# Kernel tuning notes

Measured on AMD Instinct MI355X. Metric: run time of the kernel, lower is better.

## Reference

```python
import jax, jax.numpy as jnp
import numpy as np

B, S, D = 2, 2048, 1024
H, DH = 16, 64
INNER = H * DH  # 1024
FF = 4 * D
WINDOW = 128
EPS = 1e-5
SCALE = DH ** -0.5


def setup_inputs() -> dict:
    key = jax.random.key(0)
    ks = jax.random.split(key, 8)
    s = lambda fan_in: 1.0 / np.sqrt(fan_in)
    return {
        "x": jax.random.normal(ks[0], (B, S, D), dtype=jnp.float32),
        "ln1_g": jnp.ones((D,), jnp.float32),
        "ln1_b": jnp.zeros((D,), jnp.float32),
        "w_qkv": jax.random.uniform(ks[1], (3 * INNER, D), jnp.float32, -s(D), s(D)),
        "w_out": jax.random.uniform(ks[2], (D, INNER), jnp.float32, -s(INNER), s(INNER)),
        "b_out": jnp.zeros((D,), jnp.float32),
        "ln2_g": jnp.ones((D,), jnp.float32),
        "ln2_b": jnp.zeros((D,), jnp.float32),
        "w_ff1": jax.random.uniform(ks[3], (FF, D), jnp.float32, -s(D), s(D)),
        "b_ff1": jnp.zeros((FF,), jnp.float32),
        "w_ff2": jax.random.uniform(ks[4], (D, FF), jnp.float32, -s(FF), s(FF)),
        "b_ff2": jnp.zeros((D,), jnp.float32),
    }


def _layernorm(x, g, b):
    mu = jnp.mean(x, axis=-1, keepdims=True)
    var = jnp.mean(jnp.square(x - mu), axis=-1, keepdims=True)
    return (x - mu) * jax.lax.rsqrt(var + EPS) * g + b


def reference(x, ln1_g, ln1_b, w_qkv, w_out, b_out, ln2_g, ln2_b, w_ff1, b_ff1, w_ff2, b_ff2):
    # --- attention block ---
    residual = x
    h = _layernorm(x, ln1_g, ln1_b)
    qkv = h @ w_qkv.T                             # [B, S, 3*INNER]
    q, k, v = jnp.split(qkv, 3, axis=-1)
    reshape_heads = lambda t: t.reshape(B, S, H, DH).transpose(0, 2, 1, 3)  # [B,H,S,DH]
    q, k, v = map(reshape_heads, (q, k, v))
    q = q * SCALE
    scores = jnp.einsum("bhqd,bhkd->bhqk", q, k)  # dense [B,H,S,S]
    # local sparse pattern: attend iff |i-j| <= window_size
    idx = jnp.arange(S)
    local_mask = jnp.abs(idx[:, None] - idx[None, :]) <= WINDOW  # [S,S] bool
    scores = jnp.where(local_mask[None, None], scores, -jnp.inf)
    attn = jax.nn.softmax(scores, axis=-1)
    attn = jnp.nan_to_num(attn, nan=0.0)
    out = jnp.einsum("bhqk,bhkd->bhqd", attn, v)  # [B,H,S,DH]
    out = out.transpose(0, 2, 1, 3).reshape(B, S, INNER)
    out = out @ w_out.T + b_out                   # dropout inactive (eval)
    x = residual + out
    # --- FFN block ---
    residual = x
    h = _layernorm(x, ln2_g, ln2_b)
    h = jax.nn.gelu(h @ w_ff1.T + b_ff1, approximate=False)
    h = h @ w_ff2.T + b_ff2
    return residual + h
```

## Files before the change

kernel.cpp:

```cpp
#include <hip/hip_runtime.h>
#include <stdint.h>

#define SEQ    2048
#define NB     2
#define DMODEL 1024
#define NHEAD  16
#define HDIM   64
#define FFDIM  4096
#define WIN    128
#define MTOK   (NB*SEQ)

typedef short short8 __attribute__((ext_vector_type(8)));
typedef float f32x4  __attribute__((ext_vector_type(4)));

__device__ __forceinline__ float bf2f(uint16_t h){ return __uint_as_float(((uint32_t)h) << 16); }
__device__ __forceinline__ uint16_t f2bf(float f){
  uint32_t u = __float_as_uint(f);
  u += 0x7fffu + ((u >> 16) & 1u);
  return (uint16_t)(u >> 16);
}

__device__ __forceinline__ float gelu_f(float v){
  float u = 0.7978845608028654f * v * (1.0f + 0.044715f * v * v);
  u = fminf(fmaxf(u, -10.0f), 10.0f);
  const float e = __expf(2.0f * u);
  const float th = (e - 1.0f) / (e + 1.0f);
  return 0.5f * v * (1.0f + th);
}

__device__ __forceinline__ void gl_lds16(const void* g, void* l) {
  __builtin_amdgcn_global_load_lds((const __attribute__((address_space(1))) void*)g,
                                   (__attribute__((address_space(3))) void*)l, 16, 0, 0);
}

__device__ __forceinline__ void BAR() {
  __builtin_amdgcn_s_barrier();
  __builtin_amdgcn_sched_barrier(0);
}

__global__ __launch_bounds__(256) void cvtln_kernel(
    const float* __restrict__ s0, const float* __restrict__ s1,
    const float* __restrict__ s2, const float* __restrict__ s3,
    uint16_t* __restrict__ d0, uint16_t* __restrict__ d1,
    uint16_t* __restrict__ d2, uint16_t* __restrict__ d3,
    const float* __restrict__ x, const float* __restrict__ g,
    const float* __restrict__ b, uint16_t* __restrict__ y)
{
  __shared__ float red[8];
  const int t = threadIdx.x;
  if (blockIdx.x < 12288) {
    size_t i = (size_t)blockIdx.x * 256 + t;
    const float* s; uint16_t* d; size_t off;
    if      (i <  768*1024) { s = s0; d = d0; off = i; }
    else if (i < 1024*1024) { s = s1; d = d1; off = i -  768*1024; }
    else if (i < 2048*1024) { s = s2; d = d2; off = i - 1024*1024; }
    else                    { s = s3; d = d3; off = i - 2048*1024; }
    const float4 v = ((const float4*)s)[off];
    uint2 o;
    o.x = (uint32_t)f2bf(v.x) | ((uint32_t)f2bf(v.y) << 16);
    o.y = (uint32_t)f2bf(v.z) | ((uint32_t)f2bf(v.w) << 16);
    ((uint2*)d)[off] = o;
  } else {
    const int row = blockIdx.x - 12288;
    const float4 v = ((const float4*)(x + (size_t)row * DMODEL))[t];
    float s1 = v.x + v.y + v.z + v.w;
    float s2 = v.x*v.x + v.y*v.y + v.z*v.z + v.w*v.w;
    #pragma unroll
    for (int off = 32; off; off >>= 1) { s1 += __shfl_xor(s1, off, 64); s2 += __shfl_xor(s2, off, 64); }
    const int w = t >> 6;
    if ((t & 63) == 0) { red[w] = s1; red[4+w] = s2; }
    __syncthreads();
    s1 = red[0]+red[1]+red[2]+red[3];
    s2 = red[4]+red[5]+red[6]+red[7];
    const float mu = s1 * (1.0f/DMODEL);
    const float var = s2 * (1.0f/DMODEL) - mu*mu;
    const float rs = rsqrtf(var + 1e-5f);
    const float4 gv = ((const float4*)g)[t];
    const float4 bv = ((const float4*)b)[t];
    uint2 o;
    o.x = (uint32_t)f2bf((v.x-mu)*rs*gv.x + bv.x) | ((uint32_t)f2bf((v.y-mu)*rs*gv.y + bv.y) << 16);
    o.y = (uint32_t)f2bf((v.z-mu)*rs*gv.z + bv.z) | ((uint32_t)f2bf((v.w-mu)*rs*gv.w + bv.w) << 16);
    ((uint2*)(y + (size_t)row * DMODEL))[t] = o;
  }
}

__global__ __launch_bounds__(256) void ln_kernel(const float* __restrict__ x,
                                                 const float* __restrict__ g,
                                                 const float* __restrict__ b,
                                                 uint16_t* __restrict__ y)
{
  const int row = blockIdx.x;
  const int t = threadIdx.x;
  const float4 v = ((const float4*)(x + (size_t)row * DMODEL))[t];
  float s1 = v.x + v.y + v.z + v.w;
  float s2 = v.x*v.x + v.y*v.y + v.z*v.z + v.w*v.w;
  #pragma unroll
  for (int off = 32; off; off >>= 1) { s1 += __shfl_xor(s1, off, 64); s2 += __shfl_xor(s2, off, 64); }
  __shared__ float red[8];
  const int w = t >> 6;
  if ((t & 63) == 0) { red[w] = s1; red[4+w] = s2; }
  __syncthreads();
  s1 = red[0]+red[1]+red[2]+red[3];
  s2 = red[4]+red[5]+red[6]+red[7];
  const float mu = s1 * (1.0f/DMODEL);
  const float var = s2 * (1.0f/DMODEL) - mu*mu;
  const float rs = rsqrtf(var + 1e-5f);
  const float4 gv = ((const float4*)g)[t];
  const float4 bv = ((const float4*)b)[t];
  uint2 o;
  o.x = (uint32_t)f2bf((v.x-mu)*rs*gv.x + bv.x) | ((uint32_t)f2bf((v.y-mu)*rs*gv.y + bv.y) << 16);
  o.y = (uint32_t)f2bf((v.z-mu)*rs*gv.z + bv.z) | ((uint32_t)f2bf((v.w-mu)*rs*gv.w + bv.w) << 16);
  ((uint2*)(y + (size_t)row * DMODEL))[t] = o;
}

template<int EPI>
__global__ __launch_bounds__(512, 2) void gemm256(
    const uint16_t* __restrict__ A, const uint16_t* __restrict__ Bm,
    const float* __restrict__ bias, uint16_t* __restrict__ C,
    uint16_t* __restrict__ vt, int M, int N, int K)
{
  __shared__ __align__(16) uint16_t L[4 * 16384];
  const int t = threadIdx.x;
  const int l = t & 63;
  const int w = t >> 6;
  const int wm = w >> 2, wn = w & 3;
  const int row0 = blockIdx.y * 256, col0 = blockIdx.x * 256;
  const int mrow = l & 15, kq = l >> 4;
  const int nt = K >> 5;

  f32x4 acc[8][4];
  #pragma unroll
  for (int i = 0; i < 8; ++i)
    #pragma unroll
    for (int j = 0; j < 4; ++j)
      #pragma unroll
      for (int e = 0; e < 4; ++e) acc[i][j][e] = 0.0f;

  const int sr = t >> 2;
  const int kl = (t & 3) ^ ((t >> 3) & 3);
  const uint16_t* aG = A  + (size_t)(row0 + sr) * K + kl * 8;
  const uint16_t* bG = Bm + (size_t)(col0 + sr) * K + kl * 8;
  char* const lds = (char*)L;
  const int soff = t * 16;

  #define STAGE_A(tt_) { char* d_ = lds + ((tt_) & 3) * 32768 + soff; \
      gl_lds16(aG + (tt_) * 32, d_); \
      gl_lds16(aG + (size_t)128 * K + (tt_) * 32, d_ + 8192); }
  #define STAGE_B(tt_) { char* d_ = lds + ((tt_) & 3) * 32768 + 16384 + soff; \
      gl_lds16(bG + (tt_) * 32, d_); \
      gl_lds16(bG + (size_t)128 * K + (tt_) * 32, d_ + 8192); }

  STAGE_A(0); STAGE_B(0);
  STAGE_A(1); STAGE_B(1);
  STAGE_A(2); STAGE_B(2);
  asm volatile("s_waitcnt vmcnt(8)");
  BAR();

  const int cphys = (kq ^ ((mrow >> 1) & 3)) << 4;

  for (int tt = 0; tt < nt; ++tt) {
    char* const bufA = lds + (tt & 3) * 32768;
    char* const bufB = bufA + 16384;
    short8 bf[4], af[4];
    #pragma unroll
    for (int ni = 0; ni < 4; ++ni)
      bf[ni] = *(const short8*)(bufB + (wn*64 + ni*16 + mrow) * 64 + cphys);
    #pragma unroll
    for (int mi = 0; mi < 4; ++mi)
      af[mi] = *(const short8*)(bufA + (wm*128 + mi*16 + mrow) * 64 + cphys);
    if (tt + 3 < nt) STAGE_A(tt + 3);
    BAR();
    __builtin_amdgcn_s_setprio(1);
    #pragma unroll
    for (int mi = 0; mi < 4; ++mi)
      #pragma unroll
      for (int ni = 0; ni < 4; ++ni)
        acc[mi][ni] = __builtin_amdgcn_mfma_f32_16x16x32_bf16(af[mi], bf[ni], acc[mi][ni], 0, 0, 0);
    __builtin_amdgcn_s_setprio(0);
    BAR();
    #pragma unroll
    for (int mi = 0; mi < 4; ++mi)
      af[mi] = *(const short8*)(bufA + (wm*128 + (mi+4)*16 + mrow) * 64 + cphys);
    if (tt + 3 < nt) {
      STAGE_B(tt + 3);
      asm volatile("s_waitcnt vmcnt(8)");
    } else if (tt + 3 == nt) {
      asm volatile("s_waitcnt vmcnt(4)");
    } else if (tt + 2 == nt) {
      asm volatile("s_waitcnt vmcnt(0)");
    }
    BAR();
    __builtin_amdgcn_s_setprio(1);
    #pragma unroll
    for (int mi = 0; mi < 4; ++mi)
      #pragma unroll
      for (int ni = 0; ni < 4; ++ni)
        acc[mi+4][ni] = __builtin_amdgcn_mfma_f32_16x16x32_bf16(af[mi], bf[ni], acc[mi+4][ni], 0, 0, 0);
    __builtin_amdgcn_s_setprio(0);
    BAR();
  }
  #undef STAGE_A
  #undef STAGE_B

  const int crow = kq * 4;
  if (EPI == 1 && col0 >= 2048) {
    const int hd0 = col0 - 2048 + wn*64 + mrow;
    #pragma unroll
    for (int mi = 0; mi < 8; ++mi) {
      #pragma unroll
      for (int r = 0; r < 4; ++r) {
        const int row = row0 + wm*128 + mi*16 + crow + r;
        const int bb = row >> 11, ss = row & 2047;
        uint16_t* vr = vt + ((size_t)bb << 21) + ss;
        #pragma unroll
        for (int ni = 0; ni < 4; ++ni)
          vr[(size_t)(hd0 + ni*16) << 11] = f2bf(acc[mi][ni][r]);
      }
    }
  } else {
    float bv[4];
    #pragma unroll
    for (int ni = 0; ni < 4; ++ni)
      bv[ni] = (EPI == 2) ? bias[col0 + wn*64 + ni*16 + mrow] : 0.0f;
    #pragma unroll
    for (int mi = 0; mi < 8; ++mi) {
      #pragma unroll
      for (int r = 0; r < 4; ++r) {
        const int row = row0 + wm*128 + mi*16 + crow + r;
        uint16_t* Cr = C + (size_t)row * N + col0 + wn*64 + mrow;
        #pragma unroll
        for (int ni = 0; ni < 4; ++ni) {
          float v = acc[mi][ni][r] + bv[ni];
          if (EPI == 2) v = gelu_f(v);
          Cr[ni*16] = f2bf(v);
        }
      }
    }
  }
}

__global__ __launch_bounds__(512, 2) void gemm128r(
    const uint16_t* __restrict__ A, const uint16_t* __restrict__ Bm,
    const float* __restrict__ bias, const float* __restrict__ res,
    float* __restrict__ out, int M, int N, int K)
{
  __shared__ __align__(16) uint16_t L[4 * 16384];
  const int t = threadIdx.x;
  const int l = t & 63;
  const int w = t >> 6;
  const int wm = w >> 2, wn = w & 3;
  const int row0 = blockIdx.x * 128, col0 = blockIdx.y * 128;
  const int mrow = l & 15, kq = l >> 4;
  const int nt = K >> 6;

  f32x4 acc[4][2];
  #pragma unroll
  for (int i = 0; i < 4; ++i)
    #pragma unroll
    for (int j = 0; j < 2; ++j)
      #pragma unroll
      for (int e = 0; e < 4; ++e) acc[i][j][e] = 0.0f;

  const int sr = t >> 3;
  const int kl = (t & 7) ^ (sr & 7);
  const uint16_t* aG = A  + (size_t)(row0 + sr) * K + kl * 8;
  const uint16_t* bG = Bm + (size_t)(col0 + sr) * K + kl * 8;
  char* const lds = (char*)L;
  const int soff = t * 16;

  #define STAGE_A(tt_) { char* d_ = lds + ((tt_) & 3) * 32768 + soff; \
      gl_lds16(aG + (tt_) * 64, d_); \
      gl_lds16(aG + (size_t)64 * K + (tt_) * 64, d_ + 8192); }
  #define STAGE_B(tt_) { char* d_ = lds + ((tt_) & 3) * 32768 + 16384 + soff; \
      gl_lds16(bG + (tt_) * 64, d_); \
      gl_lds16(bG + (size_t)64 * K + (tt_) * 64, d_ + 8192); }

  STAGE_A(0); STAGE_B(0);
  STAGE_A(1); STAGE_B(1);
  STAGE_A(2); STAGE_B(2);
  asm volatile("s_waitcnt vmcnt(8)");
  BAR();

  for (int tt = 0; tt < nt; ++tt) {
    char* const bufA = lds + (tt & 3) * 32768;
    char* const bufB = bufA + 16384;
    {
      const int pa = (kq ^ (mrow & 7)) * 16;
      short8 af[4], bf[2];
      #pragma unroll
      for (int ni = 0; ni < 2; ++ni)
        bf[ni] = *(const short8*)(bufB + (wn*32 + ni*16 + mrow) * 128 + pa);
      #pragma unroll
      for (int mi = 0; mi < 4; ++mi)
        af[mi] = *(const short8*)(bufA + (wm*64 + mi*16 + mrow) * 128 + pa);
      if (tt + 3 < nt) STAGE_A(tt + 3);
      BAR();
      __builtin_amdgcn_s_setprio(1);
      #pragma unroll
      for (int mi = 0; mi < 4; ++mi)
        #pragma unroll
        for (int ni = 0; ni < 2; ++ni)
          acc[mi][ni] = __builtin_amdgcn_mfma_f32_16x16x32_bf16(af[mi], bf[ni], acc[mi][ni], 0, 0, 0);
      __builtin_amdgcn_s_setprio(0);
      BAR();
    }
    {
      const int pa = ((4 + kq) ^ (mrow & 7)) * 16;
      short8 af[4], bf[2];
      #pragma unroll
      for (int ni = 0; ni < 2; ++ni)
        bf[ni] = *(const short8*)(bufB + (wn*32 + ni*16 + mrow) * 128 + pa);
      #pragma unroll
      for (int mi = 0; mi < 4; ++mi)
        af[mi] = *(const short8*)(bufA + (wm*64 + mi*16 + mrow) * 128 + pa);
      if (tt + 3 < nt) {
        STAGE_B(tt + 3);
        asm volatile("s_waitcnt vmcnt(8)");
      } else if (tt + 3 == nt) {
        asm volatile("s_waitcnt vmcnt(4)");
      } else if (tt + 2 == nt) {
        asm volatile("s_waitcnt vmcnt(0)");
      }
      BAR();
      __builtin_amdgcn_s_setprio(1);
      #pragma unroll
      for (int mi = 0; mi < 4; ++mi)
        #pragma unroll
        for (int ni = 0; ni < 2; ++ni)
          acc[mi][ni] = __builtin_amdgcn_mfma_f32_16x16x32_bf16(af[mi], bf[ni], acc[mi][ni], 0, 0, 0);
      __builtin_amdgcn_s_setprio(0);
      BAR();
    }
  }
  #undef STAGE_A
  #undef STAGE_B

  const int crow = kq * 4;
  float bv[2];
  #pragma unroll
  for (int ni = 0; ni < 2; ++ni)
    bv[ni] = bias[col0 + wn*32 + ni*16 + mrow];
  #pragma unroll
  for (int mi = 0; mi < 4; ++mi)
    #pragma unroll
    for (int r = 0; r < 4; ++r) {
      const int row = row0 + wm*64 + mi*16 + crow + r;
      const size_t base = (size_t)row * N + col0 + wn*32 + mrow;
      #pragma unroll
      for (int ni = 0; ni < 2; ++ni)
        out[base + ni*16] = acc[mi][ni][r] + bv[ni] + res[base + ni*16];
    }
}

#define TQ    32
#define NKT   18
#define NKP   288
#define PSTR  296

__global__ __launch_bounds__(256) void attn_kernel(const uint16_t* __restrict__ qkv,
                                                   const uint16_t* __restrict__ vtg,
                                                   uint16_t* __restrict__ out)
{
  __shared__ __align__(16) uint16_t Qc[8*32*8];
  __shared__ __align__(16) uint16_t Kc[8*288*8];
  __shared__ __align__(16) uint16_t Vc[36*64*8];
  const int t = threadIdx.x, l = t & 63, w = t >> 6;
  const int b = blockIdx.z, hh = blockIdx.y, q0 = blockIdx.x * TQ;
  const int k0 = (q0 - WIN > 0) ? (q0 - WIN) : 0;
  const int kend_ = q0 + TQ + WIN;
  const int kend = (kend_ < SEQ) ? kend_ : SEQ;
  const int nk = kend - k0;

  {
    const size_t vbase = ((size_t)(b*NHEAD + hh) << 17);
    #pragma unroll
    for (int i = 0; i < 9; ++i) {
      const int s = i*256 + t;
      const int c = s >> 6, d = s & 63;
      int off = k0 + c*8; if (off > 2040) off = 2040;
      gl_lds16(vtg + vbase + ((size_t)d << 11) + off, (char*)Vc + (size_t)s*16);
    }
    #pragma unroll
    for (int i = 0; i < 9; ++i) {
      const int s = i*256 + t;
      const int c = s / 288;
      const int j = s - c*288;
      const int js = (j < nk) ? j : (nk - 1);
      gl_lds16(qkv + (size_t)(b*SEQ + k0 + js)*3072 + 1024 + hh*64 + c*8,
               (char*)Kc + (size_t)s*16);
    }
    gl_lds16(qkv + (size_t)(b*SEQ + q0 + (t & 31))*3072 + hh*64 + (t >> 5)*8,
             (char*)Qc + (size_t)t*16);
  }
  __syncthreads();

  const int mrow = l & 15, q4 = l >> 4;
  f32x4 cacc[NKT];
  if (w < 2) {
    const int rb = w * 16;
    const short8 aq0 = *(const short8*)((const char*)Qc + (((q4    )*32 + rb + mrow) << 4));
    const short8 aq1 = *(const short8*)((const char*)Qc + (((4 + q4)*32 + rb + mrow) << 4));
    #pragma unroll
    for (int ct = 0; ct < NKT; ++ct) {
      f32x4 c; c[0]=0.f; c[1]=0.f; c[2]=0.f; c[3]=0.f;
      const short8 b0 = *(const short8*)((const char*)Kc + (((q4    )*288 + ct*16 + mrow) << 4));
      const short8 b1 = *(const short8*)((const char*)Kc + (((4 + q4)*288 + ct*16 + mrow) << 4));
      c = __builtin_amdgcn_mfma_f32_16x16x32_bf16(aq0, b0, c, 0, 0, 0);
      c = __builtin_amdgcn_mfma_f32_16x16x32_bf16(aq1, b1, c, 0, 0, 0);
      cacc[ct] = c;
    }
    #pragma unroll
    for (int r = 0; r < 4; ++r) {
      const int iq = q0 + rb + q4*4 + r;
      float m = -1e30f;
      #pragma unroll
      for (int ct = 0; ct < NKT; ++ct) {
        const int jj = ct*16 + mrow;
        const int j = k0 + jj;
        const bool ok = (jj < nk) && (j >= iq - WIN) && (j <= iq + WIN);
        const float s = ok ? cacc[ct][r] * 0.125f : -1e30f;
        cacc[ct][r] = s;
        m = fmaxf(m, s);
      }
      m = fmaxf(m, __shfl_xor(m, 1, 64));
      m = fmaxf(m, __shfl_xor(m, 2, 64));
      m = fmaxf(m, __shfl_xor(m, 4, 64));
      m = fmaxf(m, __shfl_xor(m, 8, 64));
      float s = 0.f;
      #pragma unroll
      for (int ct = 0; ct < NKT; ++ct) {
        const float e = __expf(cacc[ct][r] - m);
        cacc[ct][r] = e;
        s += e;
      }
      s += __shfl_xor(s, 1, 64);
      s += __shfl_xor(s, 2, 64);
      s += __shfl_xor(s, 4, 64);
      s += __shfl_xor(s, 8, 64);
      const float rinv = 1.0f / s;
      #pragma unroll
      for (int ct = 0; ct < NKT; ++ct)
        cacc[ct][r] *= rinv;
    }
  }
  __syncthreads();

  if (w < 2) {
    uint16_t* Ps = Kc;
    const int rb = w * 16;
    #pragma unroll
    for (int r = 0; r < 4; ++r)
      #pragma unroll
      for (int ct = 0; ct < NKT; ++ct)
        Ps[(rb + q4*4 + r) * PSTR + ct*16 + mrow] = f2bf(cacc[ct][r]);
  }
  __syncthreads();

  {
    const uint16_t* Ps = Kc;
    const int rt = w & 1, dt0 = (w >> 1) * 2;
    f32x4 o0, o1;
    #pragma unroll
    for (int e = 0; e < 4; ++e) { o0[e] = 0.f; o1[e] = 0.f; }
    #pragma unroll
    for (int ks = 0; ks < 9; ++ks) {
      const short8 a  = *(const short8*)((const char*)Ps + (rt*16 + mrow)*(PSTR*2) + ks*64 + q4*16);
      const short8 v0 = *(const short8*)((const char*)Vc + (((ks*4 + q4)*64 + dt0*16 + mrow) << 4));
      const short8 v1 = *(const short8*)((const char*)Vc + (((ks*4 + q4)*64 + (dt0+1)*16 + mrow) << 4));
      o0 = __builtin_amdgcn_mfma_f32_16x16x32_bf16(a, v0, o0, 0, 0, 0);
      o1 = __builtin_amdgcn_mfma_f32_16x16x32_bf16(a, v1, o1, 0, 0, 0);
    }
    #pragma unroll
    for (int r = 0; r < 4; ++r) {
      const int iq = q0 + rt*16 + q4*4 + r;
      const size_t rowoff = (size_t)(b*SEQ + iq) * DMODEL + hh*64;
      out[rowoff + (dt0  )*16 + mrow] = f2bf(o0[r]);
      out[rowoff + (dt0+1)*16 + mrow] = f2bf(o1[r]);
    }
  }
}

extern "C" void kernel_launch(void* const* d_in, const int* in_sizes, int n_in,
                              void* d_out, int out_size, void* d_ws, size_t ws_size,
                              hipStream_t stream)
{
  const float* x    = (const float*)d_in[0];
  const float* ln1g = (const float*)d_in[1];
  const float* ln1b = (const float*)d_in[2];
  const float* wqkv = (const float*)d_in[3];
  const float* wout = (const float*)d_in[4];
  const float* bout = (const float*)d_in[5];
  const float* ln2g = (const float*)d_in[6];
  const float* ln2b = (const float*)d_in[7];
  const float* wff1 = (const float*)d_in[8];
  const float* bff1 = (const float*)d_in[9];
  const float* wff2 = (const float*)d_in[10];
  const float* bff2 = (const float*)d_in[11];
  float* out = (float*)d_out;

  char* ws = (char*)d_ws;
  const size_t MB = (size_t)1 << 20;
  uint16_t* Wqkv = (uint16_t*)(ws);
  uint16_t* Wout = (uint16_t*)(ws +  6*MB);
  uint16_t* Wff1 = (uint16_t*)(ws +  8*MB);
  uint16_t* Wff2 = (uint16_t*)(ws + 16*MB);
  uint16_t* QKV  = (uint16_t*)(ws + 24*MB);
  uint16_t* H1   = (uint16_t*)(ws + 48*MB);
  uint16_t* AT   = H1;
  float*    X2f  = (float*)   (ws + 56*MB);
  uint16_t* H2   = (uint16_t*)(ws + 72*MB);
  uint16_t* FF1  = (uint16_t*)(ws + 24*MB);
  uint16_t* VT   = (uint16_t*)(ws + 80*MB);

  cvtln_kernel<<<16384, 256, 0, stream>>>(wqkv, wout, wff1, wff2,
                                          Wqkv, Wout, Wff1, Wff2,
                                          x, ln1g, ln1b, H1);
  gemm256<1><<<dim3(3072/256, MTOK/256), 512, 0, stream>>>(H1, Wqkv, nullptr, QKV, VT, MTOK, 3072, DMODEL);
  attn_kernel<<<dim3(SEQ/TQ, NHEAD, NB), 256, 0, stream>>>(QKV, VT, AT);
  gemm128r<<<dim3(MTOK/128, DMODEL/128), 512, 0, stream>>>(AT, Wout, bout, x, X2f, MTOK, DMODEL, DMODEL);
  ln_kernel<<<MTOK, 256, 0, stream>>>(X2f, ln2g, ln2b, H2);
  gemm256<2><<<dim3(FFDIM/256, MTOK/256), 512, 0, stream>>>(H2, Wff1, bff1, FF1, nullptr, MTOK, FFDIM, DMODEL);
  gemm128r<<<dim3(MTOK/128, DMODEL/128), 512, 0, stream>>>(FF1, Wff2, bff2, X2f, out, MTOK, DMODEL, FFDIM);
}
```

Measured before the change: 308.5 us.

## Software-pipeline LDS fragment loads one half-step ahead in both GEMM kernels

```diff
diff --git a/kernel.cpp b/kernel.cpp
--- a/kernel.cpp
+++ b/kernel.cpp
@@ -158,32 +158,26 @@
 
   const int cphys = (kq ^ ((mrow >> 1) & 3)) << 4;
 
+  short8 afA[4], bfc[4], afB[4], afA_n[4], bf_n[4];
+  {
+    char* const bufA = lds;
+    char* const bufB = lds + 16384;
+    #pragma unroll
+    for (int ni = 0; ni < 4; ++ni)
+      bfc[ni] = *(const short8*)(bufB + (wn*64 + ni*16 + mrow) * 64 + cphys);
+    #pragma unroll
+    for (int mi = 0; mi < 4; ++mi)
+      afA[mi] = *(const short8*)(bufA + (wm*128 + mi*16 + mrow) * 64 + cphys);
+  }
+
   for (int tt = 0; tt < nt; ++tt) {
     char* const bufA = lds + (tt & 3) * 32768;
-    char* const bufB = bufA + 16384;
-    short8 bf[4], af[4];
-    #pragma unroll
-    for (int ni = 0; ni < 4; ++ni)
-      bf[ni] = *(const short8*)(bufB + (wn*64 + ni*16 + mrow) * 64 + cphys);
-    #pragma unroll
-    for (int mi = 0; mi < 4; ++mi)
-      af[mi] = *(const short8*)(bufA + (wm*128 + mi*16 + mrow) * 64 + cphys);
-    if (tt + 3 < nt) STAGE_A(tt + 3);
-    BAR();
-    __builtin_amdgcn_s_setprio(1);
-    #pragma unroll
-    for (int mi = 0; mi < 4; ++mi)
-      #pragma unroll
-      for (int ni = 0; ni < 4; ++ni)
-        acc[mi][ni] = __builtin_amdgcn_mfma_f32_16x16x32_bf16(af[mi], bf[ni], acc[mi][ni], 0, 0, 0);
-    __builtin_amdgcn_s_setprio(0);
-    BAR();
-    #pragma unroll
-    for (int mi = 0; mi < 4; ++mi)
-      af[mi] = *(const short8*)(bufA + (wm*128 + (mi+4)*16 + mrow) * 64 + cphys);
+    #pragma unroll
+    for (int mi = 0; mi < 4; ++mi)
+      afB[mi] = *(const short8*)(bufA + (wm*128 + (mi+4)*16 + mrow) * 64 + cphys);
     if (tt + 3 < nt) {
-      STAGE_B(tt + 3);
-      asm volatile("s_waitcnt vmcnt(8)");
+      STAGE_A(tt + 3);
+      asm volatile("s_waitcnt vmcnt(6)");
     } else if (tt + 3 == nt) {
       asm volatile("s_waitcnt vmcnt(4)");
     } else if (tt + 2 == nt) {
@@ -195,9 +189,34 @@
     for (int mi = 0; mi < 4; ++mi)
       #pragma unroll
       for (int ni = 0; ni < 4; ++ni)
-        acc[mi+4][ni] = __builtin_amdgcn_mfma_f32_16x16x32_bf16(af[mi], bf[ni], acc[mi+4][ni], 0, 0, 0);
+        acc[mi][ni] = __builtin_amdgcn_mfma_f32_16x16x32_bf16(afA[mi], bfc[ni], acc[mi][ni], 0, 0, 0);
     __builtin_amdgcn_s_setprio(0);
     BAR();
+    {
+      const int nx = (tt + 1 < nt) ? (tt + 1) : tt;
+      char* const nA = lds + (nx & 3) * 32768;
+      char* const nB = nA + 16384;
+      #pragma unroll
+      for (int ni = 0; ni < 4; ++ni)
+        bf_n[ni] = *(const short8*)(nB + (wn*64 + ni*16 + mrow) * 64 + cphys);
+      #pragma unroll
+      for (int mi = 0; mi < 4; ++mi)
+        afA_n[mi] = *(const short8*)(nA + (wm*128 + mi*16 + mrow) * 64 + cphys);
+    }
+    if (tt + 3 < nt) STAGE_B(tt + 3);
+    BAR();
+    __builtin_amdgcn_s_setprio(1);
+    #pragma unroll
+    for (int mi = 0; mi < 4; ++mi)
+      #pragma unroll
+      for (int ni = 0; ni < 4; ++ni)
+        acc[mi+4][ni] = __builtin_amdgcn_mfma_f32_16x16x32_bf16(afB[mi], bfc[ni], acc[mi+4][ni], 0, 0, 0);
+    __builtin_amdgcn_s_setprio(0);
+    BAR();
+    #pragma unroll
+    for (int mi = 0; mi < 4; ++mi) afA[mi] = afA_n[mi];
+    #pragma unroll
+    for (int ni = 0; ni < 4; ++ni) bfc[ni] = bf_n[ni];
   }
   #undef STAGE_A
   #undef STAGE_B
@@ -281,56 +300,72 @@
   asm volatile("s_waitcnt vmcnt(8)");
   BAR();
 
+  const int pa0 = (kq ^ (mrow & 7)) * 16;
+  const int pa1 = ((4 + kq) ^ (mrow & 7)) * 16;
+
+  short8 af0[4], bf0[2], af1[4], bf1[2], af0n[4], bf0n[2];
+  {
+    char* const bufA = lds;
+    char* const bufB = lds + 16384;
+    #pragma unroll
+    for (int ni = 0; ni < 2; ++ni)
+      bf0[ni] = *(const short8*)(bufB + (wn*32 + ni*16 + mrow) * 128 + pa0);
+    #pragma unroll
+    for (int mi = 0; mi < 4; ++mi)
+      af0[mi] = *(const short8*)(bufA + (wm*64 + mi*16 + mrow) * 128 + pa0);
+  }
+
   for (int tt = 0; tt < nt; ++tt) {
     char* const bufA = lds + (tt & 3) * 32768;
     char* const bufB = bufA + 16384;
+    #pragma unroll
+    for (int ni = 0; ni < 2; ++ni)
+      bf1[ni] = *(const short8*)(bufB + (wn*32 + ni*16 + mrow) * 128 + pa1);
+    #pragma unroll
+    for (int mi = 0; mi < 4; ++mi)
+      af1[mi] = *(const short8*)(bufA + (wm*64 + mi*16 + mrow) * 128 + pa1);
+    if (tt + 3 < nt) {
+      STAGE_A(tt + 3);
+      asm volatile("s_waitcnt vmcnt(6)");
+    } else if (tt + 3 == nt) {
+      asm volatile("s_waitcnt vmcnt(4)");
+    } else if (tt + 2 == nt) {
+      asm volatile("s_waitcnt vmcnt(0)");
+    }
+    BAR();
+    __builtin_amdgcn_s_setprio(1);
+    #pragma unroll
+    for (int mi = 0; mi < 4; ++mi)
+      #pragma unroll
+      for (int ni = 0; ni < 2; ++ni)
+        acc[mi][ni] = __builtin_amdgcn_mfma_f32_16x16x32_bf16(af0[mi], bf0[ni], acc[mi][ni], 0, 0, 0);
+    __builtin_amdgcn_s_setprio(0);
+    BAR();
     {
-      const int pa = (kq ^ (mrow & 7)) * 16;
-      short8 af[4], bf[2];
+      const int nx = (tt + 1 < nt) ? (tt + 1) : tt;
+      char* const nA = lds + (nx & 3) * 32768;
+      char* const nB = nA + 16384;
       #pragma unroll
       for (int ni = 0; ni < 2; ++ni)
-        bf[ni] = *(const short8*)(bufB + (wn*32 + ni*16 + mrow) * 128 + pa);
+        bf0n[ni] = *(const short8*)(nB + (wn*32 + ni*16 + mrow) * 128 + pa0);
       #pragma unroll
       for (int mi = 0; mi < 4; ++mi)
-        af[mi] = *(const short8*)(bufA + (wm*64 + mi*16 + mrow) * 128 + pa);
-      if (tt + 3 < nt) STAGE_A(tt + 3);
-      BAR();
-      __builtin_amdgcn_s_setprio(1);
-      #pragma unroll
-      for (int mi = 0; mi < 4; ++mi)
-        #pragma unroll
-        for (int ni = 0; ni < 2; ++ni)
-          acc[mi][ni] = __builtin_amdgcn_mfma_f32_16x16x32_bf16(af[mi], bf[ni], acc[mi][ni], 0, 0, 0);
-      __builtin_amdgcn_s_setprio(0);
-      BAR();
-    }
-    {
-      const int pa = ((4 + kq) ^ (mrow & 7)) * 16;
-      short8 af[4], bf[2];
+        af0n[mi] = *(const short8*)(nA + (wm*64 + mi*16 + mrow) * 128 + pa0);
+    }
+    if (tt + 3 < nt) STAGE_B(tt + 3);
+    BAR();
+    __builtin_amdgcn_s_setprio(1);
+    #pragma unroll
+    for (int mi = 0; mi < 4; ++mi)
       #pragma unroll
       for (int ni = 0; ni < 2; ++ni)
-        bf[ni] = *(const short8*)(bufB + (wn*32 + ni*16 + mrow) * 128 + pa);
-      #pragma unroll
-      for (int mi = 0; mi < 4; ++mi)
-        af[mi] = *(const short8*)(bufA + (wm*64 + mi*16 + mrow) * 128 + pa);
-      if (tt + 3 < nt) {
-        STAGE_B(tt + 3);
-        asm volatile("s_waitcnt vmcnt(8)");
-      } else if (tt + 3 == nt) {
-        asm volatile("s_waitcnt vmcnt(4)");
-      } else if (tt + 2 == nt) {
-        asm volatile("s_waitcnt vmcnt(0)");
-      }
-      BAR();
-      __builtin_amdgcn_s_setprio(1);
-      #pragma unroll
-      for (int mi = 0; mi < 4; ++mi)
-        #pragma unroll
-        for (int ni = 0; ni < 2; ++ni)
-          acc[mi][ni] = __builtin_amdgcn_mfma_f32_16x16x32_bf16(af[mi], bf[ni], acc[mi][ni], 0, 0, 0);
-      __builtin_amdgcn_s_setprio(0);
-      BAR();
-    }
+        acc[mi][ni] = __builtin_amdgcn_mfma_f32_16x16x32_bf16(af1[mi], bf1[ni], acc[mi][ni], 0, 0, 0);
+    __builtin_amdgcn_s_setprio(0);
+    BAR();
+    #pragma unroll
+    for (int mi = 0; mi < 4; ++mi) af0[mi] = af0n[mi];
+    #pragma unroll
+    for (int ni = 0; ni < 2; ++ni) bf0[ni] = bf0n[ni];
   }
   #undef STAGE_A
   #undef STAGE_B
```

Measured after the change: 315.3 us. 1.02x slower.

## Merge GEMM K-loop half-steps, drop sched barriers, remap blocks across XCDs

Applied to the files above, without the earlier changes.

```diff
diff --git a/kernel.cpp b/kernel.cpp
--- a/kernel.cpp
+++ b/kernel.cpp
@@ -31,11 +31,6 @@
 __device__ __forceinline__ void gl_lds16(const void* g, void* l) {
   __builtin_amdgcn_global_load_lds((const __attribute__((address_space(1))) void*)g,
                                    (__attribute__((address_space(3))) void*)l, 16, 0, 0);
-}
-
-__device__ __forceinline__ void BAR() {
-  __builtin_amdgcn_s_barrier();
-  __builtin_amdgcn_sched_barrier(0);
 }
 
 __global__ __launch_bounds__(256) void cvtln_kernel(
@@ -124,7 +119,11 @@
   const int l = t & 63;
   const int w = t >> 6;
   const int wm = w >> 2, wn = w & 3;
-  const int row0 = blockIdx.y * 256, col0 = blockIdx.x * 256;
+  const int GX = gridDim.x;
+  const int nblk = GX * gridDim.y;
+  const int lin  = blockIdx.y * GX + blockIdx.x;
+  const int nid  = (lin & 7) * (nblk >> 3) + (lin >> 3);
+  const int row0 = (nid / GX) * 256, col0 = (nid % GX) * 256;
   const int mrow = l & 15, kq = l >> 4;
   const int nt = K >> 5;
 
@@ -154,34 +153,22 @@
   STAGE_A(1); STAGE_B(1);
   STAGE_A(2); STAGE_B(2);
   asm volatile("s_waitcnt vmcnt(8)");
-  BAR();
+  __builtin_amdgcn_s_barrier();
 
   const int cphys = (kq ^ ((mrow >> 1) & 3)) << 4;
 
   for (int tt = 0; tt < nt; ++tt) {
     char* const bufA = lds + (tt & 3) * 32768;
     char* const bufB = bufA + 16384;
-    short8 bf[4], af[4];
+    short8 bf[4], af[8];
     #pragma unroll
     for (int ni = 0; ni < 4; ++ni)
       bf[ni] = *(const short8*)(bufB + (wn*64 + ni*16 + mrow) * 64 + cphys);
     #pragma unroll
-    for (int mi = 0; mi < 4; ++mi)
+    for (int mi = 0; mi < 8; ++mi)
       af[mi] = *(const short8*)(bufA + (wm*128 + mi*16 + mrow) * 64 + cphys);
-    if (tt + 3 < nt) STAGE_A(tt + 3);
-    BAR();
-    __builtin_amdgcn_s_setprio(1);
-    #pragma unroll
-    for (int mi = 0; mi < 4; ++mi)
-      #pragma unroll
-      for (int ni = 0; ni < 4; ++ni)
-        acc[mi][ni] = __builtin_amdgcn_mfma_f32_16x16x32_bf16(af[mi], bf[ni], acc[mi][ni], 0, 0, 0);
-    __builtin_amdgcn_s_setprio(0);
-    BAR();
-    #pragma unroll
-    for (int mi = 0; mi < 4; ++mi)
-      af[mi] = *(const short8*)(bufA + (wm*128 + (mi+4)*16 + mrow) * 64 + cphys);
     if (tt + 3 < nt) {
+      STAGE_A(tt + 3);
       STAGE_B(tt + 3);
       asm volatile("s_waitcnt vmcnt(8)");
     } else if (tt + 3 == nt) {
@@ -189,15 +176,15 @@
     } else if (tt + 2 == nt) {
       asm volatile("s_waitcnt vmcnt(0)");
     }
-    BAR();
+    __builtin_amdgcn_s_barrier();
     __builtin_amdgcn_s_setprio(1);
     #pragma unroll
-    for (int mi = 0; mi < 4; ++mi)
+    for (int mi = 0; mi < 8; ++mi)
       #pragma unroll
       for (int ni = 0; ni < 4; ++ni)
-        acc[mi+4][ni] = __builtin_amdgcn_mfma_f32_16x16x32_bf16(af[mi], bf[ni], acc[mi+4][ni], 0, 0, 0);
+        acc[mi][ni] = __builtin_amdgcn_mfma_f32_16x16x32_bf16(af[mi], bf[ni], acc[mi][ni], 0, 0, 0);
     __builtin_amdgcn_s_setprio(0);
-    BAR();
+    __builtin_amdgcn_s_barrier();
   }
   #undef STAGE_A
   #undef STAGE_B
@@ -249,7 +236,11 @@
   const int l = t & 63;
   const int w = t >> 6;
   const int wm = w >> 2, wn = w & 3;
-  const int row0 = blockIdx.x * 128, col0 = blockIdx.y * 128;
+  const int GX = gridDim.x;
+  const int nblk = GX * gridDim.y;
+  const int lin  = blockIdx.y * GX + blockIdx.x;
+  const int nid  = (lin & 7) * (nblk >> 3) + (lin >> 3);
+  const int row0 = (nid % GX) * 128, col0 = (nid / GX) * 128;
   const int mrow = l & 15, kq = l >> 4;
   const int nt = K >> 6;
 
@@ -279,58 +270,48 @@
   STAGE_A(1); STAGE_B(1);
   STAGE_A(2); STAGE_B(2);
   asm volatile("s_waitcnt vmcnt(8)");
-  BAR();
+  __builtin_amdgcn_s_barrier();
+
+  const int pa0 = (kq ^ (mrow & 7)) * 16;
+  const int pa1 = ((4 + kq) ^ (mrow & 7)) * 16;
 
   for (int tt = 0; tt < nt; ++tt) {
     char* const bufA = lds + (tt & 3) * 32768;
     char* const bufB = bufA + 16384;
-    {
-      const int pa = (kq ^ (mrow & 7)) * 16;
-      short8 af[4], bf[2];
+    short8 af0[4], bf0[2], af1[4], bf1[2];
+    #pragma unroll
+    for (int ni = 0; ni < 2; ++ni) {
+      bf0[ni] = *(const short8*)(bufB + (wn*32 + ni*16 + mrow) * 128 + pa0);
+      bf1[ni] = *(const short8*)(bufB + (wn*32 + ni*16 + mrow) * 128 + pa1);
+    }
+    #pragma unroll
+    for (int mi = 0; mi < 4; ++mi) {
+      af0[mi] = *(const short8*)(bufA + (wm*64 + mi*16 + mrow) * 128 + pa0);
+      af1[mi] = *(const short8*)(bufA + (wm*64 + mi*16 + mrow) * 128 + pa1);
+    }
+    if (tt + 3 < nt) {
+      STAGE_A(tt + 3);
+      STAGE_B(tt + 3);
+      asm volatile("s_waitcnt vmcnt(8)");
+    } else if (tt + 3 == nt) {
+      asm volatile("s_waitcnt vmcnt(4)");
+    } else if (tt + 2 == nt) {
+      asm volatile("s_waitcnt vmcnt(0)");
+    }
+    __builtin_amdgcn_s_barrier();
+    __builtin_amdgcn_s_setprio(1);
+    #pragma unroll
+    for (int mi = 0; mi < 4; ++mi)
       #pragma unroll
       for (int ni = 0; ni < 2; ++ni)
-        bf[ni] = *(const short8*)(bufB + (wn*32 + ni*16 + mrow) * 128 + pa);
-      #pragma unroll
-      for (int mi = 0; mi < 4; ++mi)
-        af[mi] = *(const short8*)(bufA + (wm*64 + mi*16 + mrow) * 128 + pa);
-      if (tt + 3 < nt) STAGE_A(tt + 3);
-      BAR();
-      __builtin_amdgcn_s_setprio(1);
-      #pragma unroll
-      for (int mi = 0; mi < 4; ++mi)
-        #pragma unroll
-        for (int ni = 0; ni < 2; ++ni)
-          acc[mi][ni] = __builtin_amdgcn_mfma_f32_16x16x32_bf16(af[mi], bf[ni], acc[mi][ni], 0, 0, 0);
-      __builtin_amdgcn_s_setprio(0);
-      BAR();
-    }
-    {
-      const int pa = ((4 + kq) ^ (mrow & 7)) * 16;
-      short8 af[4], bf[2];
+        acc[mi][ni] = __builtin_amdgcn_mfma_f32_16x16x32_bf16(af0[mi], bf0[ni], acc[mi][ni], 0, 0, 0);
+    #pragma unroll
+    for (int mi = 0; mi < 4; ++mi)
       #pragma unroll
       for (int ni = 0; ni < 2; ++ni)
-        bf[ni] = *(const short8*)(bufB + (wn*32 + ni*16 + mrow) * 128 + pa);
-      #pragma unroll
-      for (int mi = 0; mi < 4; ++mi)
-        af[mi] = *(const short8*)(bufA + (wm*64 + mi*16 + mrow) * 128 + pa);
-      if (tt + 3 < nt) {
-        STAGE_B(tt + 3);
-        asm volatile("s_waitcnt vmcnt(8)");
-      } else if (tt + 3 == nt) {
-        asm volatile("s_waitcnt vmcnt(4)");
-      } else if (tt + 2 == nt) {
-        asm volatile("s_waitcnt vmcnt(0)");
-      }
-      BAR();
-      __builtin_amdgcn_s_setprio(1);
-      #pragma unroll
-      for (int mi = 0; mi < 4; ++mi)
-        #pragma unroll
-        for (int ni = 0; ni < 2; ++ni)
-          acc[mi][ni] = __builtin_amdgcn_mfma_f32_16x16x32_bf16(af[mi], bf[ni], acc[mi][ni], 0, 0, 0);
-      __builtin_amdgcn_s_setprio(0);
-      BAR();
-    }
+        acc[mi][ni] = __builtin_amdgcn_mfma_f32_16x16x32_bf16(af1[mi], bf1[ni], acc[mi][ni], 0, 0, 0);
+    __builtin_amdgcn_s_setprio(0);
+    __builtin_amdgcn_s_barrier();
   }
   #undef STAGE_A
   #undef STAGE_B
```

Result: no change. 313.5 us (+1.6%).

## Shrink GEMM tiles and LDS buffering to raise occupancy and grid fill

Applied to the files above, without the earlier changes.

```diff
diff --git a/kernel.cpp b/kernel.cpp
--- a/kernel.cpp
+++ b/kernel.cpp
@@ -114,23 +114,23 @@
 }
 
 template<int EPI>
-__global__ __launch_bounds__(512, 2) void gemm256(
+__global__ __launch_bounds__(512, 4) void gemm256(
     const uint16_t* __restrict__ A, const uint16_t* __restrict__ Bm,
     const float* __restrict__ bias, uint16_t* __restrict__ C,
     uint16_t* __restrict__ vt, int M, int N, int K)
 {
-  __shared__ __align__(16) uint16_t L[4 * 16384];
+  __shared__ __align__(16) uint16_t L[3 * 12288];
   const int t = threadIdx.x;
   const int l = t & 63;
   const int w = t >> 6;
-  const int wm = w >> 2, wn = w & 3;
-  const int row0 = blockIdx.y * 256, col0 = blockIdx.x * 256;
+  const int wm = w >> 1, wn = w & 1;
+  const int row0 = blockIdx.y * 256, col0 = blockIdx.x * 128;
   const int mrow = l & 15, kq = l >> 4;
   const int nt = K >> 5;
 
-  f32x4 acc[8][4];
+  f32x4 acc[4][4];
   #pragma unroll
-  for (int i = 0; i < 8; ++i)
+  for (int i = 0; i < 4; ++i)
     #pragma unroll
     for (int j = 0; j < 4; ++j)
       #pragma unroll
@@ -141,34 +141,33 @@
   const uint16_t* aG = A  + (size_t)(row0 + sr) * K + kl * 8;
   const uint16_t* bG = Bm + (size_t)(col0 + sr) * K + kl * 8;
   char* const lds = (char*)L;
-  const int soff = t * 16;
-
-  #define STAGE_A(tt_) { char* d_ = lds + ((tt_) & 3) * 32768 + soff; \
-      gl_lds16(aG + (tt_) * 32, d_); \
-      gl_lds16(aG + (size_t)128 * K + (tt_) * 32, d_ + 8192); }
-  #define STAGE_B(tt_) { char* d_ = lds + ((tt_) & 3) * 32768 + 16384 + soff; \
-      gl_lds16(bG + (tt_) * 32, d_); \
-      gl_lds16(bG + (size_t)128 * K + (tt_) * 32, d_ + 8192); }
-
-  STAGE_A(0); STAGE_B(0);
-  STAGE_A(1); STAGE_B(1);
-  STAGE_A(2); STAGE_B(2);
-  asm volatile("s_waitcnt vmcnt(8)");
+
+  #define STAGE(tt_) { char* s_ = lds + ((tt_) % 3) * 24576 + t * 16; \
+      gl_lds16(aG + (tt_) * 32, s_); \
+      gl_lds16(aG + (size_t)128 * K + (tt_) * 32, s_ + 8192); \
+      gl_lds16(bG + (tt_) * 32, s_ + 16384); }
+
+  STAGE(0); STAGE(1);
+  asm volatile("s_waitcnt vmcnt(3)");
   BAR();
 
   const int cphys = (kq ^ ((mrow >> 1) & 3)) << 4;
 
   for (int tt = 0; tt < nt; ++tt) {
-    char* const bufA = lds + (tt & 3) * 32768;
-    char* const bufB = bufA + 16384;
-    short8 bf[4], af[4];
+    char* const base = lds + (tt % 3) * 24576;
+    short8 af[4], bf[4];
     #pragma unroll
     for (int ni = 0; ni < 4; ++ni)
-      bf[ni] = *(const short8*)(bufB + (wn*64 + ni*16 + mrow) * 64 + cphys);
+      bf[ni] = *(const short8*)(base + 16384 + (wn*64 + ni*16 + mrow) * 64 + cphys);
     #pragma unroll
     for (int mi = 0; mi < 4; ++mi)
-      af[mi] = *(const short8*)(bufA + (wm*128 + mi*16 + mrow) * 64 + cphys);
-    if (tt + 3 < nt) STAGE_A(tt + 3);
+      af[mi] = *(const short8*)(base + (wm*64 + mi*16 + mrow) * 64 + cphys);
+    if (tt + 2 < nt) {
+      STAGE(tt + 2);
+      asm volatile("s_waitcnt vmcnt(3)");
+    } else if (tt + 1 < nt) {
+      asm volatile("s_waitcnt vmcnt(0)");
+    }
     BAR();
     __builtin_amdgcn_s_setprio(1);
     #pragma unroll
@@ -178,38 +177,17 @@
         acc[mi][ni] = __builtin_amdgcn_mfma_f32_16x16x32_bf16(af[mi], bf[ni], acc[mi][ni], 0, 0, 0);
     __builtin_amdgcn_s_setprio(0);
     BAR();
-    #pragma unroll
-    for (int mi = 0; mi < 4; ++mi)
-      af[mi] = *(const short8*)(bufA + (wm*128 + (mi+4)*16 + mrow) * 64 + cphys);
-    if (tt + 3 < nt) {
-      STAGE_B(tt + 3);
-      asm volatile("s_waitcnt vmcnt(8)");
-    } else if (tt + 3 == nt) {
-      asm volatile("s_waitcnt vmcnt(4)");
-    } else if (tt + 2 == nt) {
-      asm volatile("s_waitcnt vmcnt(0)");
-    }
-    BAR();
-    __builtin_amdgcn_s_setprio(1);
-    #pragma unroll
-    for (int mi = 0; mi < 4; ++mi)
-      #pragma unroll
-      for (int ni = 0; ni < 4; ++ni)
-        acc[mi+4][ni] = __builtin_amdgcn_mfma_f32_16x16x32_bf16(af[mi], bf[ni], acc[mi+4][ni], 0, 0, 0);
-    __builtin_amdgcn_s_setprio(0);
-    BAR();
-  }
-  #undef STAGE_A
-  #undef STAGE_B
+  }
+  #undef STAGE
 
   const int crow = kq * 4;
   if (EPI == 1 && col0 >= 2048) {
     const int hd0 = col0 - 2048 + wn*64 + mrow;
     #pragma unroll
-    for (int mi = 0; mi < 8; ++mi) {
+    for (int mi = 0; mi < 4; ++mi) {
       #pragma unroll
       for (int r = 0; r < 4; ++r) {
-        const int row = row0 + wm*128 + mi*16 + crow + r;
+        const int row = row0 + wm*64 + mi*16 + crow + r;
         const int bb = row >> 11, ss = row & 2047;
         uint16_t* vr = vt + ((size_t)bb << 21) + ss;
         #pragma unroll
@@ -223,10 +201,10 @@
     for (int ni = 0; ni < 4; ++ni)
       bv[ni] = (EPI == 2) ? bias[col0 + wn*64 + ni*16 + mrow] : 0.0f;
     #pragma unroll
-    for (int mi = 0; mi < 8; ++mi) {
+    for (int mi = 0; mi < 4; ++mi) {
       #pragma unroll
       for (int r = 0; r < 4; ++r) {
-        const int row = row0 + wm*128 + mi*16 + crow + r;
+        const int row = row0 + wm*64 + mi*16 + crow + r;
         uint16_t* Cr = C + (size_t)row * N + col0 + wn*64 + mrow;
         #pragma unroll
         for (int ni = 0; ni < 4; ++ni) {
@@ -239,12 +217,12 @@
   }
 }
 
-__global__ __launch_bounds__(512, 2) void gemm128r(
+__global__ __launch_bounds__(512, 4) void gemm128r(
     const uint16_t* __restrict__ A, const uint16_t* __restrict__ Bm,
     const float* __restrict__ bias, const float* __restrict__ res,
     float* __restrict__ out, int M, int N, int K)
 {
-  __shared__ __align__(16) uint16_t L[4 * 16384];
+  __shared__ __align__(16) uint16_t L[2 * 16384];
   const int t = threadIdx.x;
   const int l = t & 63;
   const int w = t >> 6;
@@ -268,21 +246,19 @@
   char* const lds = (char*)L;
   const int soff = t * 16;
 
-  #define STAGE_A(tt_) { char* d_ = lds + ((tt_) & 3) * 32768 + soff; \
+  #define STAGE_A(tt_) { char* d_ = lds + ((tt_) & 1) * 32768 + soff; \
       gl_lds16(aG + (tt_) * 64, d_); \
       gl_lds16(aG + (size_t)64 * K + (tt_) * 64, d_ + 8192); }
-  #define STAGE_B(tt_) { char* d_ = lds + ((tt_) & 3) * 32768 + 16384 + soff; \
+  #define STAGE_B(tt_) { char* d_ = lds + ((tt_) & 1) * 32768 + 16384 + soff; \
       gl_lds16(bG + (tt_) * 64, d_); \
       gl_lds16(bG + (size_t)64 * K + (tt_) * 64, d_ + 8192); }
 
   STAGE_A(0); STAGE_B(0);
-  STAGE_A(1); STAGE_B(1);
-  STAGE_A(2); STAGE_B(2);
-  asm volatile("s_waitcnt vmcnt(8)");
+  asm volatile("s_waitcnt vmcnt(0)");
   BAR();
 
   for (int tt = 0; tt < nt; ++tt) {
-    char* const bufA = lds + (tt & 3) * 32768;
+    char* const bufA = lds + (tt & 1) * 32768;
     char* const bufB = bufA + 16384;
     {
       const int pa = (kq ^ (mrow & 7)) * 16;
@@ -293,7 +269,7 @@
       #pragma unroll
       for (int mi = 0; mi < 4; ++mi)
         af[mi] = *(const short8*)(bufA + (wm*64 + mi*16 + mrow) * 128 + pa);
-      if (tt + 3 < nt) STAGE_A(tt + 3);
+      if (tt + 1 < nt) STAGE_A(tt + 1);
       BAR();
       __builtin_amdgcn_s_setprio(1);
       #pragma unroll
@@ -313,12 +289,8 @@
       #pragma unroll
       for (int mi = 0; mi < 4; ++mi)
         af[mi] = *(const short8*)(bufA + (wm*64 + mi*16 + mrow) * 128 + pa);
-      if (tt + 3 < nt) {
-        STAGE_B(tt + 3);
-        asm volatile("s_waitcnt vmcnt(8)");
-      } else if (tt + 3 == nt) {
-        asm volatile("s_waitcnt vmcnt(4)");
-      } else if (tt + 2 == nt) {
+      if (tt + 1 < nt) {
+        STAGE_B(tt + 1);
         asm volatile("s_waitcnt vmcnt(0)");
       }
       BAR();
@@ -515,10 +487,10 @@
   cvtln_kernel<<<16384, 256, 0, stream>>>(wqkv, wout, wff1, wff2,
                                           Wqkv, Wout, Wff1, Wff2,
                                           x, ln1g, ln1b, H1);
-  gemm256<1><<<dim3(3072/256, MTOK/256), 512, 0, stream>>>(H1, Wqkv, nullptr, QKV, VT, MTOK, 3072, DMODEL);
+  gemm256<1><<<dim3(3072/128, MTOK/256), 512, 0, stream>>>(H1, Wqkv, nullptr, QKV, VT, MTOK, 3072, DMODEL);
   attn_kernel<<<dim3(SEQ/TQ, NHEAD, NB), 256, 0, stream>>>(QKV, VT, AT);
   gemm128r<<<dim3(MTOK/128, DMODEL/128), 512, 0, stream>>>(AT, Wout, bout, x, X2f, MTOK, DMODEL, DMODEL);
   ln_kernel<<<MTOK, 256, 0, stream>>>(X2f, ln2g, ln2b, H2);
-  gemm256<2><<<dim3(FFDIM/256, MTOK/256), 512, 0, stream>>>(H2, Wff1, bff1, FF1, nullptr, MTOK, FFDIM, DMODEL);
+  gemm256<2><<<dim3(FFDIM/128, MTOK/256), 512, 0, stream>>>(H2, Wff1, bff1, FF1, nullptr, MTOK, FFDIM, DMODEL);
   gemm128r<<<dim3(MTOK/128, DMODEL/128), 512, 0, stream>>>(FF1, Wff2, bff2, X2f, out, MTOK, DMODEL, FFDIM);
 }
```

Measured after the change: 335.3 us. 8.7% more time.
